# Performance work log

Measured on AMD Instinct MI355X. Metric: run time of the kernel, lower is better.

Reference implementation:

```python
import jax, jax.numpy as jnp
import numpy as np

N_SRC = 655362   # fine-level nodes (icosphere level 8)
N6 = 163830      # coarse nodes with 6 neighbors
N7 = 12          # coarse nodes with 7 neighbors (pentagon points)
D = 128          # feature dim


def setup_inputs() -> dict:
    key = jax.random.key(0)
    k_x, k_i6, k_i7, k_perm = jax.random.split(key, 4)
    x_in = jax.random.normal(k_x, (N_SRC, D), dtype=jnp.float32)
    indices_6 = jax.random.randint(k_i6, (N6, 6), 0, N_SRC, dtype=jnp.int64)
    indices_7 = jax.random.randint(k_i7, (N7, 7), 0, N_SRC, dtype=jnp.int64)
    # indices_target is a permutation of [0, N6+N7) in the original module
    indices_target = jax.random.permutation(k_perm, N6 + N7).astype(jnp.int64)
    weights_6 = jnp.ones((N6, 6), dtype=jnp.float32)  # nn.Parameter init = ones
    weights_7 = jnp.ones((N7, 7), dtype=jnp.float32)
    return {
        "x_in": x_in,
        "weights_6": weights_6,
        "weights_7": weights_7,
        "indices_6": indices_6,
        "indices_7": indices_7,
        "indices_target": indices_target,
    }


def reference(x_in, weights_6, weights_7, indices_6, indices_7, indices_target):
    # gather fixed-degree neighborhoods, weighted sum over neighbors
    x6 = jnp.einsum('nkd,nk->nd', x_in[indices_6], weights_6)  # [N6, D]
    x7 = jnp.einsum('nkd,nk->nd', x_in[indices_7], weights_7)  # [N7, D]
    x = jnp.concatenate([x6, x7], axis=0)                      # [N6+N7, D]
    return x[indices_target]                                   # scatter reorder
```

## Files before the change

### kernel.cpp

```cpp
#include <hip/hip_runtime.h>


constexpr int N6     = 163830;
constexpr int N7     = 12;
constexpr int N_OUT  = N6 + N7;
constexpr int D      = 128;
constexpr int LANES_PER_ROW = 32;
constexpr int BLOCK  = 256;
constexpr int ROWS_PER_BLOCK = BLOCK / LANES_PER_ROW;

__global__ __launch_bounds__(BLOCK) void pooling_kernel(
    const float* __restrict__ x_in,
    const float* __restrict__ w6,
    const float* __restrict__ w7,
    const int*   __restrict__ idx6,
    const int*   __restrict__ idx7,
    const int*   __restrict__ tgt,
    float*       __restrict__ out)
{
    const int row  = blockIdx.x * ROWS_PER_BLOCK + (threadIdx.x >> 5);
    const int lane = threadIdx.x & 31;
    if (row >= N_OUT) return;

    const int n = __builtin_nontemporal_load(tgt + row);

    float4 acc = make_float4(0.f, 0.f, 0.f, 0.f);

    if (n < N6) {
        const int*   ip = idx6 + (size_t)n * 6;
        const float* wp = w6   + (size_t)n * 6;
        int   src[6];
        float w[6];
#pragma unroll
        for (int k = 0; k < 6; ++k) {
            src[k] = __builtin_nontemporal_load(ip + k);
            w[k]   = __builtin_nontemporal_load(wp + k);
        }
#pragma unroll
        for (int k = 0; k < 6; ++k) {
            const float4 v = *reinterpret_cast<const float4*>(
                x_in + (size_t)src[k] * D + (size_t)lane * 4);
            acc.x += w[k] * v.x;
            acc.y += w[k] * v.y;
            acc.z += w[k] * v.z;
            acc.w += w[k] * v.w;
        }
    } else {
        const int m = n - N6;
        const int*   ip = idx7 + (size_t)m * 7;
        const float* wp = w7   + (size_t)m * 7;
#pragma unroll
        for (int k = 0; k < 7; ++k) {
            const int   s = __builtin_nontemporal_load(ip + k);
            const float w = __builtin_nontemporal_load(wp + k);
            const float4 v = *reinterpret_cast<const float4*>(
                x_in + (size_t)s * D + (size_t)lane * 4);
            acc.x += w * v.x;
            acc.y += w * v.y;
            acc.z += w * v.z;
            acc.w += w * v.w;
        }
    }

    float* op = out + (size_t)row * D + (size_t)lane * 4;
    __builtin_nontemporal_store(acc.x, op + 0);
    __builtin_nontemporal_store(acc.y, op + 1);
    __builtin_nontemporal_store(acc.z, op + 2);
    __builtin_nontemporal_store(acc.w, op + 3);
}

extern "C" void kernel_launch(void* const* d_in, const int* in_sizes, int n_in,
                              void* d_out, int out_size, void* d_ws, size_t ws_size,
                              hipStream_t stream) {
    const float* x_in = (const float*)d_in[0];
    const float* w6   = (const float*)d_in[1];
    const float* w7   = (const float*)d_in[2];
    const int*   idx6 = (const int*)d_in[3];
    const int*   idx7 = (const int*)d_in[4];
    const int*   tgt  = (const int*)d_in[5];
    float*       out  = (float*)d_out;

    const int grid = (N_OUT + ROWS_PER_BLOCK - 1) / ROWS_PER_BLOCK;
    pooling_kernel<<<grid, BLOCK, 0, stream>>>(x_in, w6, w7, idx6, idx7, tgt, out);
}
```

Measured before the change: 98.04 us.

## Split gather into two source-range passes with bf16 partial workspace

```diff
diff --git a/kernel.cpp b/kernel.cpp
--- a/kernel.cpp
+++ b/kernel.cpp
@@ -1,15 +1,108 @@
 #include <hip/hip_runtime.h>
 
 
-constexpr int N6     = 163830;
-constexpr int N7     = 12;
-constexpr int N_OUT  = N6 + N7;
-constexpr int D      = 128;
-constexpr int LANES_PER_ROW = 32;
-constexpr int BLOCK  = 256;
-constexpr int ROWS_PER_BLOCK = BLOCK / LANES_PER_ROW;
+constexpr int N_SRC = 655362;
+constexpr int N6    = 163830;
+constexpr int N7    = 12;
+constexpr int N_OUT = N6 + N7;
+constexpr int D     = 128;
+constexpr int CHUNK = N_SRC / 2 + 1;
 
-__global__ __launch_bounds__(BLOCK) void pooling_kernel(
+constexpr int BLOCK = 256;
+constexpr int GPB   = BLOCK / 32;
+constexpr int GRID_ROWS = (N_OUT + GPB - 1) / GPB;
+
+__device__ __forceinline__ unsigned short f2bf(float f) {
+    unsigned u = __builtin_bit_cast(unsigned, f);
+    unsigned r = (u + 0x7FFFu + ((u >> 16) & 1u)) >> 16;
+    return (unsigned short)r;
+}
+__device__ __forceinline__ float bf2f(unsigned short h) {
+    unsigned u = ((unsigned)h) << 16;
+    return __builtin_bit_cast(float, u);
+}
+
+template <int PHASE, int DEG>
+__device__ __forceinline__ float4 gather_row(const float* __restrict__ x_in,
+                                             const int* __restrict__ ip,
+                                             const float* __restrict__ wp,
+                                             int lane) {
+    int   se[DEG];
+    float we[DEG];
+#pragma unroll
+    for (int k = 0; k < DEG; ++k) {
+        const int   s = ip[k];
+        const float w = wp[k];
+        const bool  c = (PHASE == 0) ? (s < CHUNK) : (s >= CHUNK);
+        se[k] = c ? s : 0;
+        we[k] = c ? w : 0.f;
+    }
+    float4 v[DEG];
+#pragma unroll
+    for (int k = 0; k < DEG; ++k)
+        v[k] = *reinterpret_cast<const float4*>(
+            x_in + (size_t)se[k] * D + lane * 4);
+    float4 a = make_float4(0.f, 0.f, 0.f, 0.f);
+#pragma unroll
+    for (int k = 0; k < DEG; ++k) {
+        a.x += we[k] * v[k].x;
+        a.y += we[k] * v[k].y;
+        a.z += we[k] * v[k].z;
+        a.w += we[k] * v[k].w;
+    }
+    return a;
+}
+
+template <int PHASE>
+__global__ __launch_bounds__(BLOCK) void pool_phase_kernel(
+    const float* __restrict__ x_in,
+    const float* __restrict__ w6,
+    const float* __restrict__ w7,
+    const int*   __restrict__ idx6,
+    const int*   __restrict__ idx7,
+    const int*   __restrict__ tgt,
+    unsigned short* __restrict__ part,
+    float*       __restrict__ out)
+{
+    const int row  = blockIdx.x * GPB + (threadIdx.x >> 5);
+    const int lane = threadIdx.x & 31;
+    if (row >= N_OUT) return;
+
+    const int n = tgt[row];
+
+    ushort4 pin;
+    if (PHASE == 1)
+        pin = *reinterpret_cast<const ushort4*>(part + (size_t)row * D + lane * 4);
+
+    float4 acc;
+    if (n < N6) {
+        acc = gather_row<PHASE, 6>(x_in, idx6 + 6 * (size_t)n,
+                                   w6 + 6 * (size_t)n, lane);
+    } else {
+        const int m = n - N6;
+        acc = gather_row<PHASE, 7>(x_in, idx7 + 7 * (size_t)m,
+                                   w7 + 7 * (size_t)m, lane);
+    }
+
+    if (PHASE == 0) {
+        ushort4 p;
+        p.x = f2bf(acc.x); p.y = f2bf(acc.y);
+        p.z = f2bf(acc.z); p.w = f2bf(acc.w);
+        *reinterpret_cast<ushort4*>(part + (size_t)row * D + lane * 4) = p;
+    } else {
+        acc.x += bf2f(pin.x);
+        acc.y += bf2f(pin.y);
+        acc.z += bf2f(pin.z);
+        acc.w += bf2f(pin.w);
+        float* op = out + (size_t)row * D + lane * 4;
+        __builtin_nontemporal_store(acc.x, op + 0);
+        __builtin_nontemporal_store(acc.y, op + 1);
+        __builtin_nontemporal_store(acc.z, op + 2);
+        __builtin_nontemporal_store(acc.w, op + 3);
+    }
+}
+
+__global__ __launch_bounds__(BLOCK) void pool_simple_kernel(
     const float* __restrict__ x_in,
     const float* __restrict__ w6,
     const float* __restrict__ w7,
@@ -18,51 +111,36 @@
     const int*   __restrict__ tgt,
     float*       __restrict__ out)
 {
-    const int row  = blockIdx.x * ROWS_PER_BLOCK + (threadIdx.x >> 5);
+    const int row  = blockIdx.x * GPB + (threadIdx.x >> 5);
     const int lane = threadIdx.x & 31;
     if (row >= N_OUT) return;
-
-    const int n = __builtin_nontemporal_load(tgt + row);
-
+    const int n = tgt[row];
     float4 acc = make_float4(0.f, 0.f, 0.f, 0.f);
-
     if (n < N6) {
-        const int*   ip = idx6 + (size_t)n * 6;
-        const float* wp = w6   + (size_t)n * 6;
-        int   src[6];
-        float w[6];
+        const int*   ip = idx6 + 6 * (size_t)n;
+        const float* wp = w6   + 6 * (size_t)n;
 #pragma unroll
         for (int k = 0; k < 6; ++k) {
-            src[k] = __builtin_nontemporal_load(ip + k);
-            w[k]   = __builtin_nontemporal_load(wp + k);
-        }
-#pragma unroll
-        for (int k = 0; k < 6; ++k) {
+            const float w  = wp[k];
             const float4 v = *reinterpret_cast<const float4*>(
-                x_in + (size_t)src[k] * D + (size_t)lane * 4);
-            acc.x += w[k] * v.x;
-            acc.y += w[k] * v.y;
-            acc.z += w[k] * v.z;
-            acc.w += w[k] * v.w;
+                x_in + (size_t)ip[k] * D + lane * 4);
+            acc.x += w * v.x; acc.y += w * v.y;
+            acc.z += w * v.z; acc.w += w * v.w;
         }
     } else {
         const int m = n - N6;
-        const int*   ip = idx7 + (size_t)m * 7;
-        const float* wp = w7   + (size_t)m * 7;
+        const int*   ip = idx7 + 7 * (size_t)m;
+        const float* wp = w7   + 7 * (size_t)m;
 #pragma unroll
         for (int k = 0; k < 7; ++k) {
-            const int   s = __builtin_nontemporal_load(ip + k);
-            const float w = __builtin_nontemporal_load(wp + k);
+            const float w  = wp[k];
             const float4 v = *reinterpret_cast<const float4*>(
-                x_in + (size_t)s * D + (size_t)lane * 4);
-            acc.x += w * v.x;
-            acc.y += w * v.y;
-            acc.z += w * v.z;
-            acc.w += w * v.w;
+                x_in + (size_t)ip[k] * D + lane * 4);
+            acc.x += w * v.x; acc.y += w * v.y;
+            acc.z += w * v.z; acc.w += w * v.w;
         }
     }
-
-    float* op = out + (size_t)row * D + (size_t)lane * 4;
+    float* op = out + (size_t)row * D + lane * 4;
     __builtin_nontemporal_store(acc.x, op + 0);
     __builtin_nontemporal_store(acc.y, op + 1);
     __builtin_nontemporal_store(acc.z, op + 2);
@@ -80,6 +158,15 @@
     const int*   tgt  = (const int*)d_in[5];
     float*       out  = (float*)d_out;
 
-    const int grid = (N_OUT + ROWS_PER_BLOCK - 1) / ROWS_PER_BLOCK;
-    pooling_kernel<<<grid, BLOCK, 0, stream>>>(x_in, w6, w7, idx6, idx7, tgt, out);
+    const size_t part_bytes = (size_t)N_OUT * D * sizeof(unsigned short);
+    if (ws_size >= part_bytes) {
+        unsigned short* part = (unsigned short*)d_ws;
+        pool_phase_kernel<0><<<GRID_ROWS, BLOCK, 0, stream>>>(
+            x_in, w6, w7, idx6, idx7, tgt, part, out);
+        pool_phase_kernel<1><<<GRID_ROWS, BLOCK, 0, stream>>>(
+            x_in, w6, w7, idx6, idx7, tgt, part, out);
+    } else {
+        pool_simple_kernel<<<GRID_ROWS, BLOCK, 0, stream>>>(
+            x_in, w6, w7, idx6, idx7, tgt, out);
+    }
 }
```

Measured after the change: 109.7 us. 1.12x slower.
